# Performance work log

Measured on AMD Instinct MI355X. Metric: run time of the kernel, lower is better.

## Reference

```python
import jax, jax.numpy as jnp
import numpy as np

ALPHA = 0.2  # LeakyReLU negative slope

def setup_inputs() -> dict:
    key = jax.random.key(0)
    k1, k2, k3 = jax.random.split(key, 3)
    N, F_in, F_out = 8192, 128, 64
    h = jax.random.normal(k1, (N, F_in), dtype=jnp.float32)
    W = jax.random.normal(k2, (F_in, F_out), dtype=jnp.float32) * 0.1
    a = jax.random.normal(k3, (2 * F_out, 1), dtype=jnp.float32) * 0.1
    return {"h": h, "W": W, "a": a}

def reference(h, W, a):
    # Wh: [N, F_out]
    Wh = h @ W
    F_out = Wh.shape[1]
    # Split 'a' into source/dest halves; e_ij = leakyrelu(a1.Wh_i + a2.Wh_j)
    a1 = a[:F_out, 0]   # [F_out]
    a2 = a[F_out:, 0]   # [F_out]
    e_src = Wh @ a1     # [N]
    e_dst = Wh @ a2     # [N]
    e = e_src[:, None] + e_dst[None, :]          # [N, N]
    e = jnp.where(e > 0, e, ALPHA * e)           # leaky relu
    attention = jax.nn.softmax(e, axis=1)        # dropout omitted (eval mode)
    h_prime = attention @ Wh                     # [N, F_out]
    return jax.nn.elu(h_prime)                   # concat=True path
```

## Files before the change

kernel.cpp:

```cpp
#include <hip/hip_runtime.h>


typedef unsigned long long ull;

constexpr int N_ROWS = 8192;
constexpr int F_IN   = 128;
constexpr int F_OUT  = 64;
#define LRELU_ALPHA 0.2f

constexpr int SBLK = 8;
constexpr int NGRP = N_ROWS / SBLK;

constexpr int WS_WH   = 0;
constexpr int WS_ESRC = WS_WH + N_ROWS * F_OUT;
constexpr int WS_KEYA = WS_ESRC + N_ROWS;
constexpr int WS_KEYB = WS_KEYA + 2 * N_ROWS;
constexpr int WS_GS1T = WS_KEYB + 2 * N_ROWS;
constexpr int WS_GS2T = WS_GS1T + F_OUT * NGRP;
constexpr int WS_GD1  = WS_GS2T + F_OUT * NGRP;
constexpr int WS_GD2  = WS_GD1 + NGRP;
constexpr int WS_P1   = WS_GD2 + NGRP;
constexpr int WS_P2   = WS_P1 + (NGRP + 1) * F_OUT;
constexpr int WS_D1   = WS_P2 + (NGRP + 1) * F_OUT;
constexpr int WS_D2   = WS_D1 + (NGRP + 1);
static_assert((WS_KEYA % 2) == 0 && (WS_KEYB % 2) == 0, "keys 8B-aligned");

__device__ __forceinline__ unsigned mono_enc(float f) {
  unsigned u = __float_as_uint(f);
  return u ^ ((u & 0x80000000u) ? 0xFFFFFFFFu : 0x80000000u);
}
__device__ __forceinline__ float mono_dec(unsigned e) {
  unsigned u = e ^ ((e & 0x80000000u) ? 0x80000000u : 0xFFFFFFFFu);
  return __uint_as_float(u);
}

__global__ __launch_bounds__(256) void k1_wh(const float* __restrict__ h,
                                             const float* __restrict__ W,
                                             const float* __restrict__ a,
                                             float* __restrict__ ws) {
  __shared__ float hlds[16 * F_IN];
  __shared__ float alds[2 * F_OUT];
  const int t = threadIdx.x;
  const int row0 = blockIdx.x * 16;

  const float4* hsrc = (const float4*)(h + (long)row0 * F_IN);
  float4* hd = (float4*)hlds;
  hd[t]       = hsrc[t];
  hd[t + 256] = hsrc[t + 256];
  if (t < 2 * F_OUT) alds[t] = a[t];
  __syncthreads();

  const int wave = t >> 6, lane = t & 63;
  const float* hp = hlds + (wave * 4) * F_IN;
  float acc0 = 0.f, acc1 = 0.f, acc2 = 0.f, acc3 = 0.f;

  #pragma unroll 4
  for (int k4 = 0; k4 < F_IN; k4 += 4) {
    float4 h0 = *(const float4*)(hp + k4);
    float4 h1 = *(const float4*)(hp + F_IN + k4);
    float4 h2 = *(const float4*)(hp + 2 * F_IN + k4);
    float4 h3 = *(const float4*)(hp + 3 * F_IN + k4);
    float w0 = W[(k4 + 0) * F_OUT + lane];
    float w1 = W[(k4 + 1) * F_OUT + lane];
    float w2 = W[(k4 + 2) * F_OUT + lane];
    float w3 = W[(k4 + 3) * F_OUT + lane];
    acc0 = fmaf(h0.x, w0, acc0); acc0 = fmaf(h0.y, w1, acc0);
    acc0 = fmaf(h0.z, w2, acc0); acc0 = fmaf(h0.w, w3, acc0);
    acc1 = fmaf(h1.x, w0, acc1); acc1 = fmaf(h1.y, w1, acc1);
    acc1 = fmaf(h1.z, w2, acc1); acc1 = fmaf(h1.w, w3, acc1);
    acc2 = fmaf(h2.x, w0, acc2); acc2 = fmaf(h2.y, w1, acc2);
    acc2 = fmaf(h2.z, w2, acc2); acc2 = fmaf(h2.w, w3, acc2);
    acc3 = fmaf(h3.x, w0, acc3); acc3 = fmaf(h3.y, w1, acc3);
    acc3 = fmaf(h3.z, w2, acc3); acc3 = fmaf(h3.w, w3, acc3);
  }

  const int grow = row0 + wave * 4;
  float* Wh = ws + WS_WH;
  Wh[(grow + 0) * F_OUT + lane] = acc0;
  Wh[(grow + 1) * F_OUT + lane] = acc1;
  Wh[(grow + 2) * F_OUT + lane] = acc2;
  Wh[(grow + 3) * F_OUT + lane] = acc3;

  const float a1 = alds[lane], a2 = alds[F_OUT + lane];
  float s0 = acc0 * a1, s1 = acc1 * a1, s2 = acc2 * a1, s3 = acc3 * a1;
  float d0 = acc0 * a2, d1 = acc1 * a2, d2 = acc2 * a2, d3 = acc3 * a2;
  #pragma unroll
  for (int off = 32; off; off >>= 1) {
    s0 += __shfl_down(s0, off); s1 += __shfl_down(s1, off);
    s2 += __shfl_down(s2, off); s3 += __shfl_down(s3, off);
    d0 += __shfl_down(d0, off); d1 += __shfl_down(d1, off);
    d2 += __shfl_down(d2, off); d3 += __shfl_down(d3, off);
  }
  if (lane == 0) {
    ws[WS_ESRC + grow + 0] = s0; ws[WS_ESRC + grow + 1] = s1;
    ws[WS_ESRC + grow + 2] = s2; ws[WS_ESRC + grow + 3] = s3;
    ull* keys = (ull*)(ws + WS_KEYA);
    keys[grow + 0] = ((ull)mono_enc(d0) << 32) | (unsigned)(grow + 0);
    keys[grow + 1] = ((ull)mono_enc(d1) << 32) | (unsigned)(grow + 1);
    keys[grow + 2] = ((ull)mono_enc(d2) << 32) | (unsigned)(grow + 2);
    keys[grow + 3] = ((ull)mono_enc(d3) << 32) | (unsigned)(grow + 3);
  }
}

__global__ __launch_bounds__(1024) void k2a_1024(ull* __restrict__ keys) {
  __shared__ ull lk[1024];
  const int t = threadIdx.x;
  const int base = blockIdx.x * 1024;
  lk[t] = keys[base + t];
  __syncthreads();
  for (int k = 2; k <= 1024; k <<= 1) {
    for (int j = k >> 1; j > 0; j >>= 1) {
      int p = t ^ j;
      if (p > t) {
        ull x = lk[t], y = lk[p];
        bool asc = ((t & k) == 0);
        if ((x > y) == asc) { lk[t] = y; lk[p] = x; }
      }
      __syncthreads();
    }
  }
  keys[base + t] = lk[t];
}

__global__ __launch_bounds__(512) void k2_rank(const ull* __restrict__ src,
                                               ull* __restrict__ dst) {
  __shared__ ull lk[8192];
  const int t = threadIdx.x;
  #pragma unroll
  for (int c = 0; c < 16; ++c) lk[c * 512 + t] = src[c * 512 + t];
  __syncthreads();

  const int g = blockIdx.x * 512 + t;
  const ull key = lk[g];
  const int myrun = g >> 10;
  int pos = g & 1023;

  #pragma unroll
  for (int r = 0; r < 8; ++r) {
    if (r == myrun) continue;
    const ull* base = lk + (r << 10);
    int p = 0;
    #pragma unroll
    for (int step = 512; step >= 1; step >>= 1)
      p += (base[p + step - 1] < key) ? step : 0;
    p += (base[p] < key) ? 1 : 0;
    pos += p;
  }
  dst[pos] = key;
}

__global__ __launch_bounds__(1024) void k3_tables(float* __restrict__ ws) {
  __shared__ float sa[1024];
  __shared__ float sb[1024];
  const int t = threadIdx.x;
  const int blk = blockIdx.x;
  const ull* K = (const ull*)(ws + WS_KEYB);
  const float* Wh = ws + WS_WH;

  float s1 = 0.f, s2 = 0.f;
  if (blk < 64) {
    const int c = blk;
    const ull* kp = K + (t << 3);
    #pragma unroll
    for (int o = 0; o < SBLK; ++o) {
      ull key = kp[o];
      float d = mono_dec((unsigned)(key >> 32));
      int j = (int)(key & 0xFFFFFFFFu);
      float e1 = __expf(d), e2 = __expf(LRELU_ALPHA * d);
      float v = Wh[j * F_OUT + c];
      s1 = fmaf(e1, v, s1); s2 = fmaf(e2, v, s2);
    }
  } else {
    const ull* kp = K + (t << 3);
    #pragma unroll
    for (int o = 0; o < SBLK; ++o) {
      ull key = kp[o];
      float d = mono_dec((unsigned)(key >> 32));
      s1 += __expf(d); s2 += __expf(LRELU_ALPHA * d);
    }
  }

  const float xa = s1, xb = s2;
  sa[t] = xa; sb[t] = xb;
  __syncthreads();
  for (int off = 1; off < 1024; off <<= 1) {
    float ya = (t >= off) ? sa[t - off] : 0.f;
    float yb = (t >= off) ? sb[t - off] : 0.f;
    __syncthreads();
    sa[t] += ya; sb[t] += yb;
    __syncthreads();
  }
  const float ia = sa[t], ib = sb[t];
  const float ea = ia - xa, eb = ib - xb;

  if (blk < 64) {
    const int c = blk;
    ws[WS_P1 + t * F_OUT + c] = ea;
    ws[WS_P2 + t * F_OUT + c] = eb;
    if (t == NGRP - 1) {
      ws[WS_P1 + NGRP * F_OUT + c] = ia;
      ws[WS_P2 + NGRP * F_OUT + c] = ib;
    }
  } else {
    ws[WS_D1 + t] = ea;
    ws[WS_D2 + t] = eb;
    if (t == NGRP - 1) {
      ws[WS_D1 + NGRP] = ia;
      ws[WS_D2 + NGRP] = ib;
    }
  }
}

__global__ __launch_bounds__(256) void k4_out(const float* __restrict__ ws,
                                              float* __restrict__ out) {
  const int t = threadIdx.x, wv = t >> 6, lane = t & 63;
  const int i = blockIdx.x * 4 + wv;
  const ull* K = (const ull*)(ws + WS_KEYB);
  const float s = ws[WS_ESRC + i];
  const float ns = (s == 0.0f) ? 0.0f : -s;
  const unsigned Ki = mono_enc(ns);

  unsigned m1 = (unsigned)(K[lane << 7] >> 32);
  ull bal1 = __ballot(m1 <= Ki);
  int tl;
  if (bal1 == 0ull) {
    tl = 0;
  } else {
    int L1 = 63 - __clzll((long long)bal1);
    int base = L1 << 7;
    unsigned m2 = (unsigned)(K[base + (lane << 1)] >> 32);
    ull bal2 = __ballot(m2 <= Ki);
    int L2 = 63 - __clzll((long long)bal2);
    int p = base + (L2 << 1) + 1;
    unsigned m3 = (unsigned)(K[p] >> 32);
    tl = p + ((m3 <= Ki) ? 1 : 0);
  }
  const int b = tl >> 3, rr = tl & 7;

  float p1 = ws[WS_P1 + b * F_OUT + lane];
  float p2 = ws[WS_P2 + b * F_OUT + lane];
  float d1 = ws[WS_D1 + b], d2 = ws[WS_D2 + b];
  const float p1tot = ws[WS_P1 + NGRP * F_OUT + lane];
  const float d1tot = ws[WS_D1 + NGRP];
  const float* Wh = ws + WS_WH;

  for (int o = 0; o < rr; ++o) {
    ull key = K[(b << 3) + o];
    float d = mono_dec((unsigned)(key >> 32));
    int j = (int)(key & 0xFFFFFFFFu);
    float e1 = __expf(d), e2 = __expf(LRELU_ALPHA * d);
    float v = Wh[j * F_OUT + lane];
    p1 = fmaf(e1, v, p1); p2 = fmaf(e2, v, p2);
    d1 += e1; d2 += e2;
  }

  const float es1 = __expf(s), es2 = __expf(LRELU_ALPHA * s);
  const float num = es1 * (p1tot - p1) + es2 * p2;
  const float den = es1 * (d1tot - d1) + es2 * d2;
  const float r = num / den;
  out[i * F_OUT + lane] = (r > 0.f) ? r : (__expf(r) - 1.f);
}

extern "C" void kernel_launch(void* const* d_in, const int* in_sizes, int n_in,
                              void* d_out, int out_size, void* d_ws, size_t ws_size,
                              hipStream_t stream) {
  const float* h = (const float*)d_in[0];
  const float* W = (const float*)d_in[1];
  const float* a = (const float*)d_in[2];
  float* ws = (float*)d_ws;
  float* out = (float*)d_out;
  ull* keyA = (ull*)(ws + WS_KEYA);
  ull* keyB = (ull*)(ws + WS_KEYB);

  hipLaunchKernelGGL(k1_wh,     dim3(N_ROWS / 16), dim3(256),  0, stream, h, W, a, ws);
  hipLaunchKernelGGL(k2a_1024,  dim3(8),           dim3(1024), 0, stream, keyA);
  hipLaunchKernelGGL(k2_rank,   dim3(16),          dim3(512),  0, stream, keyA, keyB);
  hipLaunchKernelGGL(k3_tables, dim3(65),          dim3(1024), 0, stream, ws);
  hipLaunchKernelGGL(k4_out,    dim3(N_ROWS / 4),  dim3(256),  0, stream, ws, out);
}
```

Baseline: 99.69 us.

## Replace bitonic sort plus merge-rank with parallel brute-force rank counting

Removes the two-kernel sort (per-1024 bitonic sort in 8 blocks, then merge-rank in 16 blocks) and replaces it with one kernel. Sixteen lanes cooperatively count how many of all 8192 keys are smaller than each key, then scatter it to its rank. This trades O(N^2) comparisons for far more parallelism across 256 blocks and one fewer launch and barrier-heavy phase. Each block reloads the full 64 KB key array into LDS, which adds global/L2 traffic.

```diff
diff --git a/kernel.cpp b/kernel.cpp
--- a/kernel.cpp
+++ b/kernel.cpp
@@ -102,51 +102,34 @@
   }
 }
 
-__global__ __launch_bounds__(1024) void k2a_1024(ull* __restrict__ keys) {
-  __shared__ ull lk[1024];
-  const int t = threadIdx.x;
-  const int base = blockIdx.x * 1024;
-  lk[t] = keys[base + t];
-  __syncthreads();
-  for (int k = 2; k <= 1024; k <<= 1) {
-    for (int j = k >> 1; j > 0; j >>= 1) {
-      int p = t ^ j;
-      if (p > t) {
-        ull x = lk[t], y = lk[p];
-        bool asc = ((t & k) == 0);
-        if ((x > y) == asc) { lk[t] = y; lk[p] = x; }
-      }
-      __syncthreads();
-    }
-  }
-  keys[base + t] = lk[t];
-}
-
-__global__ __launch_bounds__(512) void k2_rank(const ull* __restrict__ src,
+__global__ __launch_bounds__(512) void k2_sort(const ull* __restrict__ src,
                                                ull* __restrict__ dst) {
   __shared__ ull lk[8192];
   const int t = threadIdx.x;
+
+  ulonglong2* lkv = (ulonglong2*)lk;
+  const ulonglong2* srcv = (const ulonglong2*)src;
   #pragma unroll
-  for (int c = 0; c < 16; ++c) lk[c * 512 + t] = src[c * 512 + t];
+  for (int c = 0; c < 8; ++c) lkv[c * 512 + t] = srcv[c * 512 + t];
   __syncthreads();
 
-  const int g = blockIdx.x * 512 + t;
-  const ull key = lk[g];
-  const int myrun = g >> 10;
-  int pos = g & 1023;
-
-  #pragma unroll
-  for (int r = 0; r < 8; ++r) {
-    if (r == myrun) continue;
-    const ull* base = lk + (r << 10);
-    int p = 0;
-    #pragma unroll
-    for (int step = 512; step >= 1; step >>= 1)
-      p += (base[p + step - 1] < key) ? step : 0;
-    p += (base[p] < key) ? 1 : 0;
-    pos += p;
-  }
-  dst[pos] = key;
+  const int kidx = (blockIdx.x << 5) + (t >> 4);
+  const ull key = lk[kidx];
+  const int s = t & 15;
+
+  int cnt = 0;
+  const ulonglong2* lk2 = (const ulonglong2*)lk;
+  #pragma unroll 8
+  for (int i = 0; i < 256; ++i) {
+    ulonglong2 v = lk2[(i << 4) | s];
+    cnt += (v.x < key) ? 1 : 0;
+    cnt += (v.y < key) ? 1 : 0;
+  }
+  cnt += __shfl_down(cnt, 8, 16);
+  cnt += __shfl_down(cnt, 4, 16);
+  cnt += __shfl_down(cnt, 2, 16);
+  cnt += __shfl_down(cnt, 1, 16);
+  if (s == 0) dst[cnt] = key;
 }
 
 __global__ __launch_bounds__(1024) void k3_tables(float* __restrict__ ws) {
@@ -273,8 +256,7 @@
   ull* keyB = (ull*)(ws + WS_KEYB);
 
   hipLaunchKernelGGL(k1_wh,     dim3(N_ROWS / 16), dim3(256),  0, stream, h, W, a, ws);
-  hipLaunchKernelGGL(k2a_1024,  dim3(8),           dim3(1024), 0, stream, keyA);
-  hipLaunchKernelGGL(k2_rank,   dim3(16),          dim3(512),  0, stream, keyA, keyB);
+  hipLaunchKernelGGL(k2_sort,   dim3(256),         dim3(512),  0, stream, keyA, keyB);
   hipLaunchKernelGGL(k3_tables, dim3(65),          dim3(1024), 0, stream, ws);
   hipLaunchKernelGGL(k4_out,    dim3(N_ROWS / 4),  dim3(256),  0, stream, ws, out);
 }
```

Result: faster. 93.83 us (-5.9%).
